# Optimization experiments

Measured on AMD Instinct MI355X. Metric: run time of the kernel, lower is better.

Reference implementation:

```python
import jax, jax.numpy as jnp
import numpy as np

C = 512
GROUPS = 32
EPS = 1e-6


def setup_inputs() -> dict:
    key = jax.random.key(0)
    ks = jax.random.split(key, 10)
    B, H, W = 4, 64, 64
    s = 0.02
    return {
        "x": jax.random.normal(ks[0], (B, C, H, W), dtype=jnp.float32),
        "gamma": jnp.ones((C,), jnp.float32),
        "beta": jnp.zeros((C,), jnp.float32),
        "Wq": jax.random.normal(ks[1], (C, C), jnp.float32) * s,
        "bq": jnp.zeros((C,), jnp.float32),
        "Wk": jax.random.normal(ks[2], (C, C), jnp.float32) * s,
        "bk": jnp.zeros((C,), jnp.float32),
        "Wv": jax.random.normal(ks[3], (C, C), jnp.float32) * s,
        "bv": jnp.zeros((C,), jnp.float32),
        "Wo": jax.random.normal(ks[4], (C, C), jnp.float32) * s,
        "bo": jnp.zeros((C,), jnp.float32),
    }


def _group_norm(x, gamma, beta):
    B, Cc, H, W = x.shape
    xg = x.reshape(B, GROUPS, Cc // GROUPS, H, W)
    mean = jnp.mean(xg, axis=(2, 3, 4), keepdims=True)
    var = jnp.var(xg, axis=(2, 3, 4), keepdims=True)
    xn = ((xg - mean) * jax.lax.rsqrt(var + EPS)).reshape(B, Cc, H, W)
    return xn * gamma[None, :, None, None] + beta[None, :, None, None]


def _conv1x1(x, Wm, b):
    # x: [B,C,H,W], Wm: [Cout,Cin]
    return jnp.einsum('bchw,oc->bohw', x, Wm) + b[None, :, None, None]


def reference(x, gamma, beta, Wq, bq, Wk, bk, Wv, bv, Wo, bo):
    B, Cc, H, W = x.shape
    h = _group_norm(x, gamma, beta)
    q = _conv1x1(h, Wq, bq).reshape(B, Cc, H * W)  # [B,C,N]
    k = _conv1x1(h, Wk, bk).reshape(B, Cc, H * W)
    v = _conv1x1(h, Wv, bv).reshape(B, Cc, H * W)
    scale = float(Cc) ** (-0.5)
    # attn[b,i,j] = sum_c q[b,c,i] k[b,c,j]
    attn = jnp.einsum('bci,bcj->bij', q, k) * scale
    attn = jax.nn.softmax(attn, axis=2)
    # out[b,c,i] = sum_j v[b,c,j] attn[b,i,j]
    out = jnp.einsum('bcj,bij->bci', v, attn).reshape(B, Cc, H, W)
    out = _conv1x1(out, Wo, bo)
    return x + out
```

## Files before the change

### kernel.cpp

```cpp
#include <hip/hip_runtime.h>
#include <hip/hip_bf16.h>


#define C_DIM 512
#define N_SPA 4096
#define BATCH 4
#define NALL 16384

#define BM 128
#define BN 128
#define BK 32

typedef short short8 __attribute__((ext_vector_type(8)));
typedef short short4v __attribute__((ext_vector_type(4)));
typedef float float4v __attribute__((ext_vector_type(4)));

__device__ __forceinline__ short f2b(float f) {
  __hip_bfloat16 h = __float2bfloat16(f);
  return *reinterpret_cast<short*>(&h);
}
__device__ __forceinline__ float b2f(short s) {
  __hip_bfloat16 h;
  *reinterpret_cast<short*>(&h) = s;
  return __bfloat162float(h);
}

typedef __attribute__((address_space(1))) const void gvoid_t;
typedef __attribute__((address_space(3))) void lvoid_t;
__device__ __forceinline__ void gload16(const void* g, void* l) {
  __builtin_amdgcn_global_load_lds((gvoid_t*)g, (lvoid_t*)l, 16, 0, 0);
}

__global__ void wconv_kernel(const float* __restrict__ Wq, const float* __restrict__ Wk,
                             const float* __restrict__ Wv, const float* __restrict__ Wo,
                             const float* __restrict__ bq, const float* __restrict__ bk,
                             const float* __restrict__ bv,
                             short* __restrict__ out, float* __restrict__ bias_all) {
  int i = blockIdx.x * 256 + threadIdx.x;
  out[0 * 262144 + i] = f2b(Wq[i]);
  out[1 * 262144 + i] = f2b(Wk[i]);
  out[2 * 262144 + i] = f2b(Wv[i]);
  out[3 * 262144 + i] = f2b(Wo[i]);
  if (i < 1536) bias_all[i] = (i < 512) ? bq[i] : (i < 1024) ? bk[i - 512] : bv[i - 1024];
}

__global__ void gn_part(const float* __restrict__ x, float2* __restrict__ partials) {
  int grp = blockIdx.x >> 5, split = blockIdx.x & 31;
  const float4* xg = (const float4*)(x + (size_t)grp * 65536 + split * 2048);
  int t = threadIdx.x;
  float4 a = xg[t], b4 = xg[256 + t];
  float s = a.x + a.y + a.z + a.w + b4.x + b4.y + b4.z + b4.w;
  float ss = a.x * a.x + a.y * a.y + a.z * a.z + a.w * a.w +
             b4.x * b4.x + b4.y * b4.y + b4.z * b4.z + b4.w * b4.w;
  __shared__ float red[512];
  red[t] = s; red[256 + t] = ss;
  __syncthreads();
  for (int off = 128; off > 0; off >>= 1) {
    if (t < off) { red[t] += red[t + off]; red[256 + t] += red[256 + t + off]; }
    __syncthreads();
  }
  if (t == 0) partials[blockIdx.x] = make_float2(red[0], red[256]);
}

__global__ void gn_norm(const float* __restrict__ x, const float* __restrict__ gamma,
                        const float* __restrict__ beta, const float2* __restrict__ partials,
                        short* __restrict__ h_t) {
  int bid = blockIdx.x;
  int grp = bid >> 4, seg = bid & 15;
  int b = grp >> 5, g = grp & 31;
  float s = 0.f, ss = 0.f;
  for (int j = 0; j < 32; ++j) { float2 p2 = partials[grp * 32 + j]; s += p2.x; ss += p2.y; }
  float mean = s * (1.0f / 65536.0f);
  float rstd = rsqrtf(ss * (1.0f / 65536.0f) - mean * mean + 1e-6f);

  const float* xg = x + (size_t)grp * 65536 + seg * 256;
  __shared__ float tile[16][257];
  int t = threadIdx.x;
#pragma unroll
  for (int i = 0; i < 16; ++i) tile[i][t] = xg[(size_t)i * N_SPA + t];
  __syncthreads();

  int c8 = (t & 1) * 8, ci = g * 16 + c8;
  float ga[8], be[8];
#pragma unroll
  for (int j = 0; j < 8; ++j) { ga[j] = gamma[ci + j]; be[j] = beta[ci + j]; }
#pragma unroll
  for (int pass = 0; pass < 2; ++pass) {
    int nl = (t >> 1) + pass * 128;
    short8 o;
#pragma unroll
    for (int j = 0; j < 8; ++j) {
      float v = (tile[c8 + j][nl] - mean) * rstd * ga[j] + be[j];
      o[j] = f2b(v);
    }
    *(short8*)&h_t[((size_t)b * N_SPA + seg * 256 + nl) * C_DIM + ci] = o;
  }
}

template <int EPI>
__global__ __launch_bounds__(256) void gemm_bt(
    const short* __restrict__ A, const short* __restrict__ BT, void* __restrict__ Cout,
    const float* __restrict__ bias, const float* __restrict__ resid,
    int M, int N, int K, int lda, int ldb, int ldc,
    size_t az, size_t bz, size_t cz, float scale) {
  __shared__ __align__(16) short lds_a[BM * BK];
  __shared__ __align__(16) short lds_b[BN * BK];
  int t = threadIdx.x;
  int m0 = blockIdx.y * BM;
  int n0 = blockIdx.x * BN;
  int z = blockIdx.z;
  A += (size_t)z * az;
  BT += (size_t)z * bz;
  int w = t >> 6, l = t & 63;
  int wm = (w >> 1) * 64, wn = (w & 1) * 64;
  int lr = l & 15, lk = l >> 4;

  int sr = l >> 2, scol = (l & 3) * 8;
  const short* ga0 = A + (size_t)(m0 + w * 16 + sr) * lda + scol;
  const short* ga1 = ga0 + (size_t)64 * lda;
  const short* gb0 = BT + (size_t)(n0 + w * 16 + sr) * ldb + scol;
  const short* gb1 = gb0 + (size_t)64 * ldb;
  short* la0 = &lds_a[w * 16 * BK];
  short* la1 = &lds_a[(64 + w * 16) * BK];
  short* lb0 = &lds_b[w * 16 * BK];
  short* lb1 = &lds_b[(64 + w * 16) * BK];

  float4v acc[4][4];
#pragma unroll
  for (int i = 0; i < 4; ++i)
#pragma unroll
    for (int j = 0; j < 4; ++j) acc[i][j] = (float4v){0.f, 0.f, 0.f, 0.f};

  for (int k0 = 0; k0 < K; k0 += BK) {
    __syncthreads();
    gload16(ga0, la0); gload16(ga1, la1);
    gload16(gb0, lb0); gload16(gb1, lb1);
    ga0 += BK; ga1 += BK; gb0 += BK; gb1 += BK;
    __syncthreads();
    short8 af[4], bf[4];
#pragma unroll
    for (int i = 0; i < 4; ++i) af[i] = *(const short8*)&lds_a[(wm + i * 16 + lr) * BK + lk * 8];
#pragma unroll
    for (int i = 0; i < 4; ++i) bf[i] = *(const short8*)&lds_b[(wn + i * 16 + lr) * BK + lk * 8];
#pragma unroll
    for (int i = 0; i < 4; ++i)
#pragma unroll
      for (int j = 0; j < 4; ++j)
        acc[i][j] = __builtin_amdgcn_mfma_f32_16x16x32_bf16(af[i], bf[j], acc[i][j], 0, 0, 0);
  }

#pragma unroll
  for (int i = 0; i < 4; ++i)
#pragma unroll
    for (int j = 0; j < 4; ++j) {
      int mB = m0 + wm + i * 16 + lk * 4;
      int nn = n0 + wn + j * 16 + lr;
      if constexpr (EPI == 2) {
        short* outp = (short*)Cout + (size_t)z * cz;
#pragma unroll
        for (int r = 0; r < 4; ++r)
          outp[(size_t)(mB + r) * ldc + nn] = f2b(acc[i][j][r] * scale);
      } else if constexpr (EPI == 3) {
        short* outp = (short*)Cout + (size_t)z * cz;
        short4v v;
#pragma unroll
        for (int r = 0; r < 4; ++r) v[r] = f2b(acc[i][j][r]);
        *(short4v*)(outp + (size_t)nn * ldc + mB) = v;
      } else if constexpr (EPI == 4) {
        int bb = nn >> 12, n = nn & 4095;
        size_t base = ((size_t)bb * C_DIM + mB) * N_SPA + n;
#pragma unroll
        for (int r = 0; r < 4; ++r) {
          float f = acc[i][j][r] + bias[mB + r] + resid[base + (size_t)r * N_SPA];
          ((float*)Cout)[base + (size_t)r * N_SPA] = f;
        }
      } else {
        short* outp = (short*)Cout + (size_t)z * NALL * C_DIM;
        const float* bz_ = bias + (size_t)z * C_DIM;
        if (z < 2) {
          short4v v;
#pragma unroll
          for (int r = 0; r < 4; ++r) v[r] = f2b(acc[i][j][r] + bz_[mB + r]);
          *(short4v*)(outp + (size_t)nn * C_DIM + mB) = v;
        } else {
#pragma unroll
          for (int r = 0; r < 4; ++r)
            outp[(size_t)(mB + r) * NALL + nn] = f2b(acc[i][j][r] + bz_[mB + r]);
        }
      }
    }
}

__global__ void softmax_kernel(short* __restrict__ p) {
  size_t row = blockIdx.x;
  short8* pr = (short8*)(p + row * N_SPA);
  int t = threadIdx.x;
  short8 a = pr[t * 2], b = pr[t * 2 + 1];
  float v[16];
#pragma unroll
  for (int j = 0; j < 8; ++j) { v[j] = b2f(a[j]); v[8 + j] = b2f(b[j]); }
  float mx = v[0];
#pragma unroll
  for (int j = 1; j < 16; ++j) mx = fmaxf(mx, v[j]);
  __shared__ float red[256];
  red[t] = mx; __syncthreads();
  for (int off = 128; off > 0; off >>= 1) {
    if (t < off) red[t] = fmaxf(red[t], red[t + off]);
    __syncthreads();
  }
  mx = red[0];
  __syncthreads();
  float s = 0.f;
#pragma unroll
  for (int j = 0; j < 16; ++j) { v[j] = __expf(v[j] - mx); s += v[j]; }
  red[t] = s; __syncthreads();
  for (int off = 128; off > 0; off >>= 1) {
    if (t < off) red[t] += red[t + off];
    __syncthreads();
  }
  float inv = 1.0f / red[0];
  short8 oa, ob;
#pragma unroll
  for (int j = 0; j < 8; ++j) { oa[j] = f2b(v[j] * inv); ob[j] = f2b(v[8 + j] * inv); }
  pr[t * 2] = oa; pr[t * 2 + 1] = ob;
}

extern "C" void kernel_launch(void* const* d_in, const int* in_sizes, int n_in,
                              void* d_out, int out_size, void* d_ws, size_t ws_size,
                              hipStream_t stream) {
  const float* x     = (const float*)d_in[0];
  const float* gamma = (const float*)d_in[1];
  const float* beta  = (const float*)d_in[2];
  const float* Wq = (const float*)d_in[3];  const float* bq = (const float*)d_in[4];
  const float* Wk = (const float*)d_in[5];  const float* bk = (const float*)d_in[6];
  const float* Wv = (const float*)d_in[7];  const float* bv = (const float*)d_in[8];
  const float* Wo = (const float*)d_in[9];  const float* bo = (const float*)d_in[10];
  float* out = (float*)d_out;

  short* Wb  = (short*)d_ws;
  short* h_t = Wb + 4 * 262144;
  short* q_t = h_t + (size_t)NALL * C_DIM;
  short* k_t = q_t + (size_t)NALL * C_DIM;
  short* v_  = k_t + (size_t)NALL * C_DIM;
  short* p   = v_  + (size_t)NALL * C_DIM;
  float2* partials = (float2*)(p + (size_t)BATCH * N_SPA * N_SPA);
  float* bias_all = (float*)(partials + 4096);
  short* o_t = h_t;

  wconv_kernel<<<1024, 256, 0, stream>>>(Wq, Wk, Wv, Wo, bq, bk, bv, Wb, bias_all);
  gn_part<<<BATCH * 32 * 32, 256, 0, stream>>>(x, partials);
  gn_norm<<<BATCH * 32 * 16, 256, 0, stream>>>(x, gamma, beta, partials, h_t);

  const float scale = 0.04419417382415922f;
  const size_t pz = (size_t)N_SPA * N_SPA;
  const size_t hz = (size_t)N_SPA * C_DIM;

  gemm_bt<6><<<dim3(NALL / BN, C_DIM / BM, 3), 256, 0, stream>>>(
      Wb, h_t, q_t, bias_all, nullptr,
      C_DIM, NALL, C_DIM, C_DIM, C_DIM, C_DIM, 262144, 0, 0, 0.f);

  gemm_bt<2><<<dim3(N_SPA / BN, N_SPA / BM, BATCH), 256, 0, stream>>>(
      q_t, k_t, p, nullptr, nullptr,
      N_SPA, N_SPA, C_DIM, C_DIM, C_DIM, N_SPA, hz, hz, pz, scale);

  softmax_kernel<<<BATCH * N_SPA, 256, 0, stream>>>(p);

  gemm_bt<3><<<dim3(N_SPA / BN, C_DIM / BM, BATCH), 256, 0, stream>>>(
      v_, p, o_t, nullptr, nullptr,
      C_DIM, N_SPA, N_SPA, NALL, N_SPA, C_DIM, N_SPA, pz, hz, 0.f);

  gemm_bt<4><<<dim3(NALL / BN, C_DIM / BM, 1), 256, 0, stream>>>(
      Wb + 3 * 262144, o_t, out, bo, x,
      C_DIM, NALL, C_DIM, C_DIM, C_DIM, 0, 0, 0, 0, 0.f);
}
```

Before: 421.9 us.

## Split PV GEMM along K and fold partial sums into output projection

The attention-times-V GEMM is split into two K halves, each writing a bf16 partial into a doubled-width buffer. The Wo weight is duplicated along its input dimension so the final projection GEMM sums both partials during its own reduction. This doubles the block count of the long-K GEMM to improve CU occupancy. In exchange, the output projection does twice the K work and the partials are rounded to bf16 before summation.

```diff
diff --git a/kernel.cpp b/kernel.cpp
--- a/kernel.cpp
+++ b/kernel.cpp
@@ -40,7 +40,10 @@
   out[0 * 262144 + i] = f2b(Wq[i]);
   out[1 * 262144 + i] = f2b(Wk[i]);
   out[2 * 262144 + i] = f2b(Wv[i]);
-  out[3 * 262144 + i] = f2b(Wo[i]);
+  short wo = f2b(Wo[i]);
+  int r = i >> 9, c = i & 511;
+  out[3 * 262144 + r * 1024 + c] = wo;
+  out[3 * 262144 + r * 1024 + 512 + c] = wo;
   if (i < 1536) bias_all[i] = (i < 512) ? bq[i] : (i < 1024) ? bk[i - 512] : bv[i - 1024];
 }
 
@@ -109,8 +112,14 @@
   int m0 = blockIdx.y * BM;
   int n0 = blockIdx.x * BN;
   int z = blockIdx.z;
-  A += (size_t)z * az;
-  BT += (size_t)z * bz;
+  if constexpr (EPI == 5) {
+    int b = z >> 1, s = z & 1;
+    A += (size_t)b * N_SPA + (size_t)s * 2048;
+    BT += (size_t)b * N_SPA * N_SPA + (size_t)s * 2048;
+  } else {
+    A += (size_t)z * az;
+    BT += (size_t)z * bz;
+  }
   int w = t >> 6, l = t & 63;
   int wm = (w >> 1) * 64, wn = (w & 1) * 64;
   int lr = l & 15, lk = l >> 4;
@@ -160,12 +169,6 @@
 #pragma unroll
         for (int r = 0; r < 4; ++r)
           outp[(size_t)(mB + r) * ldc + nn] = f2b(acc[i][j][r] * scale);
-      } else if constexpr (EPI == 3) {
-        short* outp = (short*)Cout + (size_t)z * cz;
-        short4v v;
-#pragma unroll
-        for (int r = 0; r < 4; ++r) v[r] = f2b(acc[i][j][r]);
-        *(short4v*)(outp + (size_t)nn * ldc + mB) = v;
       } else if constexpr (EPI == 4) {
         int bb = nn >> 12, n = nn & 4095;
         size_t base = ((size_t)bb * C_DIM + mB) * N_SPA + n;
@@ -174,6 +177,12 @@
           float f = acc[i][j][r] + bias[mB + r] + resid[base + (size_t)r * N_SPA];
           ((float*)Cout)[base + (size_t)r * N_SPA] = f;
         }
+      } else if constexpr (EPI == 5) {
+        short* outp = (short*)Cout + (size_t)(z >> 1) * N_SPA * 1024 + (size_t)(z & 1) * C_DIM;
+        short4v v;
+#pragma unroll
+        for (int r = 0; r < 4; ++r) v[r] = f2b(acc[i][j][r]);
+        *(short4v*)(outp + (size_t)nn * 1024 + mB) = v;
       } else {
         short* outp = (short*)Cout + (size_t)z * NALL * C_DIM;
         const float* bz_ = bias + (size_t)z * C_DIM;
@@ -238,14 +247,14 @@
   float* out = (float*)d_out;
 
   short* Wb  = (short*)d_ws;
-  short* h_t = Wb + 4 * 262144;
+  short* h_t = Wb + 3 * 262144 + 524288;
   short* q_t = h_t + (size_t)NALL * C_DIM;
   short* k_t = q_t + (size_t)NALL * C_DIM;
   short* v_  = k_t + (size_t)NALL * C_DIM;
   short* p   = v_  + (size_t)NALL * C_DIM;
-  float2* partials = (float2*)(p + (size_t)BATCH * N_SPA * N_SPA);
+  short* o2  = p   + (size_t)BATCH * N_SPA * N_SPA;
+  float2* partials = (float2*)(o2 + (size_t)NALL * 1024);
   float* bias_all = (float*)(partials + 4096);
-  short* o_t = h_t;
 
   wconv_kernel<<<1024, 256, 0, stream>>>(Wq, Wk, Wv, Wo, bq, bk, bv, Wb, bias_all);
   gn_part<<<BATCH * 32 * 32, 256, 0, stream>>>(x, partials);
@@ -265,11 +274,11 @@
 
   softmax_kernel<<<BATCH * N_SPA, 256, 0, stream>>>(p);
 
-  gemm_bt<3><<<dim3(N_SPA / BN, C_DIM / BM, BATCH), 256, 0, stream>>>(
-      v_, p, o_t, nullptr, nullptr,
-      C_DIM, N_SPA, N_SPA, NALL, N_SPA, C_DIM, N_SPA, pz, hz, 0.f);
+  gemm_bt<5><<<dim3(N_SPA / BN, C_DIM / BM, BATCH * 2), 256, 0, stream>>>(
+      v_, p, o2, nullptr, nullptr,
+      C_DIM, N_SPA, N_SPA / 2, NALL, N_SPA, 1024, 0, 0, 0, 0.f);
 
   gemm_bt<4><<<dim3(NALL / BN, C_DIM / BM, 1), 256, 0, stream>>>(
-      Wb + 3 * 262144, o_t, out, bo, x,
-      C_DIM, NALL, C_DIM, C_DIM, C_DIM, 0, 0, 0, 0, 0.f);
-}
+      Wb + 3 * 262144, o2, out, bo, x,
+      C_DIM, NALL, 1024, 1024, 1024, 0, 0, 0, 0, 0.f);
+}
```

After: 438.8 us. +4.0%, slower.

## Fuse exp into QK GEMM and defer softmax normalization to PV epilogue

Applied to the files above, without the earlier changes.

The QK^T GEMM epilogue now stores exp(score*scale) directly. The softmax kernel becomes a read-only row-sum kernel that writes one inverse sum per row, and the PV GEMM epilogue multiplies its output by that inverse. This removes the full rewrite of the 4x4096x4096 probability matrix and the max-reduction pass. The trade-off is that dropping max subtraction risks overflow or precision loss when attention scores are large.

```diff
diff --git a/kernel.cpp b/kernel.cpp
--- a/kernel.cpp
+++ b/kernel.cpp
@@ -159,12 +159,13 @@
         short* outp = (short*)Cout + (size_t)z * cz;
 #pragma unroll
         for (int r = 0; r < 4; ++r)
-          outp[(size_t)(mB + r) * ldc + nn] = f2b(acc[i][j][r] * scale);
+          outp[(size_t)(mB + r) * ldc + nn] = f2b(__expf(acc[i][j][r] * scale));
       } else if constexpr (EPI == 3) {
         short* outp = (short*)Cout + (size_t)z * cz;
+        float inv = bias[(size_t)z * N_SPA + nn];
         short4v v;
 #pragma unroll
-        for (int r = 0; r < 4; ++r) v[r] = f2b(acc[i][j][r]);
+        for (int r = 0; r < 4; ++r) v[r] = f2b(acc[i][j][r] * inv);
         *(short4v*)(outp + (size_t)nn * ldc + mB) = v;
       } else if constexpr (EPI == 4) {
         int bb = nn >> 12, n = nn & 4095;
@@ -191,38 +192,21 @@
     }
 }
 
-__global__ void softmax_kernel(short* __restrict__ p) {
+__global__ void rowsum_kernel(const short* __restrict__ p, float* __restrict__ inv_sum) {
   size_t row = blockIdx.x;
-  short8* pr = (short8*)(p + row * N_SPA);
+  const short8* pr = (const short8*)(p + row * N_SPA);
   int t = threadIdx.x;
   short8 a = pr[t * 2], b = pr[t * 2 + 1];
-  float v[16];
-#pragma unroll
-  for (int j = 0; j < 8; ++j) { v[j] = b2f(a[j]); v[8 + j] = b2f(b[j]); }
-  float mx = v[0];
-#pragma unroll
-  for (int j = 1; j < 16; ++j) mx = fmaxf(mx, v[j]);
+  float s = 0.f;
+#pragma unroll
+  for (int j = 0; j < 8; ++j) s += b2f(a[j]) + b2f(b[j]);
   __shared__ float red[256];
-  red[t] = mx; __syncthreads();
-  for (int off = 128; off > 0; off >>= 1) {
-    if (t < off) red[t] = fmaxf(red[t], red[t + off]);
-    __syncthreads();
-  }
-  mx = red[0];
-  __syncthreads();
-  float s = 0.f;
-#pragma unroll
-  for (int j = 0; j < 16; ++j) { v[j] = __expf(v[j] - mx); s += v[j]; }
   red[t] = s; __syncthreads();
   for (int off = 128; off > 0; off >>= 1) {
     if (t < off) red[t] += red[t + off];
     __syncthreads();
   }
-  float inv = 1.0f / red[0];
-  short8 oa, ob;
-#pragma unroll
-  for (int j = 0; j < 8; ++j) { oa[j] = f2b(v[j] * inv); ob[j] = f2b(v[8 + j] * inv); }
-  pr[t * 2] = oa; pr[t * 2 + 1] = ob;
+  if (t == 0) inv_sum[row] = 1.0f / red[0];
 }
 
 extern "C" void kernel_launch(void* const* d_in, const int* in_sizes, int n_in,
@@ -243,7 +227,8 @@
   short* k_t = q_t + (size_t)NALL * C_DIM;
   short* v_  = k_t + (size_t)NALL * C_DIM;
   short* p   = v_  + (size_t)NALL * C_DIM;
-  float2* partials = (float2*)(p + (size_t)BATCH * N_SPA * N_SPA);
+  float* inv_sum = (float*)(p + (size_t)BATCH * N_SPA * N_SPA);
+  float2* partials = (float2*)(inv_sum + NALL);
   float* bias_all = (float*)(partials + 4096);
   short* o_t = h_t;
 
@@ -263,10 +248,10 @@
       q_t, k_t, p, nullptr, nullptr,
       N_SPA, N_SPA, C_DIM, C_DIM, C_DIM, N_SPA, hz, hz, pz, scale);
 
-  softmax_kernel<<<BATCH * N_SPA, 256, 0, stream>>>(p);
+  rowsum_kernel<<<NALL, 256, 0, stream>>>(p, inv_sum);
 
   gemm_bt<3><<<dim3(N_SPA / BN, C_DIM / BM, BATCH), 256, 0, stream>>>(
-      v_, p, o_t, nullptr, nullptr,
+      v_, p, o_t, inv_sum, nullptr,
       C_DIM, N_SPA, N_SPA, NALL, N_SPA, C_DIM, N_SPA, pz, hz, 0.f);
 
   gemm_bt<4><<<dim3(NALL / BN, C_DIM / BM, 1), 256, 0, stream>>>(
```

Measured after the change: 405.1 us. 1.04x faster.
